# Optimization experiments

Measured on AMD Instinct MI355X. Metric: run time of the kernel, lower is better.

Reference implementation:

```python
import jax, jax.numpy as jnp
import numpy as np

MARGIN = 0.5
AP_VALUE = 0.8
AN_VALUE = 0.4
ABS_W = 1.0


def setup_inputs() -> dict:
    key = jax.random.key(0)
    k1, k2 = jax.random.split(key)
    bs, d = 16384, 64
    inputs = jax.random.normal(k1, (bs, d), dtype=jnp.float32)
    target = jax.random.randint(k2, (bs,), 0, 64, dtype=jnp.int64)
    return {"inputs": inputs, "target": target}


def reference(inputs, target):
    # L2-normalize features (normalize_feature=True)
    x = inputs / jnp.linalg.norm(inputs, axis=-1, keepdims=True)

    # cross-entropy on normalized features treated as logits
    logp = jax.nn.log_softmax(x, axis=-1)  # [bs, d]
    loss_ce = -jnp.mean(jnp.take_along_axis(logp, target[:, None], axis=1))

    # cosine-similarity matrix [bs, bs]
    dist = x @ x.T

    is_pos = target[None, :] == target[:, None]
    # hard mining: min similarity among positives, max among negatives (per row)
    dist_ap = jnp.min(jnp.where(is_pos, dist, jnp.inf), axis=1)   # [bs]
    dist_an = jnp.max(jnp.where(is_pos, -jnp.inf, dist), axis=1)  # [bs]

    loss = jnp.mean(jax.nn.relu(MARGIN + dist_ap - dist_an))

    # absolute (angular margin) terms
    abs_ap = jax.nn.relu(AP_VALUE - dist_ap)
    abs_an = jax.nn.relu(dist_an - AN_VALUE)
    loss = (jnp.mean(abs_an) + jnp.mean(abs_ap)) * ABS_W + loss

    return loss + loss_ce
```

## Files before the change

kernel.cpp:

```cpp
#include <hip/hip_runtime.h>


#define N_ROWS 16384
#define N_DIM 64

typedef __attribute__((ext_vector_type(8))) short bf16x8;
typedef __attribute__((ext_vector_type(4))) float f32x4;

__device__ inline unsigned short f2bf(float f) {
  unsigned u = __float_as_uint(f);
  unsigned r = u + 0x7fffu + ((u >> 16) & 1u);
  return (unsigned short)(r >> 16);
}

__device__ inline unsigned enc_key(float f) {
  unsigned u = __float_as_uint(f);
  return (u & 0x80000000u) ? ~u : (u | 0x80000000u);
}
__device__ inline float dec_key(unsigned k) {
  unsigned u = (k & 0x80000000u) ? (k ^ 0x80000000u) : ~k;
  return __uint_as_float(u);
}

__device__ inline void g2lds16(const void* g, void* l) {
  __builtin_amdgcn_global_load_lds(
      (const __attribute__((address_space(1))) void*)g,
      (__attribute__((address_space(3))) void*)l, 16, 0, 0);
}

__global__ void prep_kernel(const float* __restrict__ x, const int* __restrict__ tgt,
                            unsigned short* __restrict__ xb, float* __restrict__ ce_row,
                            unsigned* __restrict__ mp_key, unsigned* __restrict__ mn_key,
                            float* __restrict__ out) {
  const int row  = blockIdx.x * 4 + (threadIdx.x >> 6);
  const int lane = threadIdx.x & 63;
  float v  = x[row * N_DIM + lane];
  float ss = v * v;
#pragma unroll
  for (int s = 1; s < 64; s <<= 1) ss += __shfl_xor(ss, s, 64);
  float xn = v * rsqrtf(ss);
  xb[row * N_DIM + lane] = f2bf(xn);

  float e  = __expf(xn);
  float se = e;
#pragma unroll
  for (int s = 1; s < 64; s <<= 1) se += __shfl_xor(se, s, 64);
  float lse = __logf(se);
  int   t   = tgt[row];
  float xt  = __shfl(xn, t, 64);
  if (lane == 0) {
    ce_row[row] = lse - xt;
    mp_key[row] = 0xFFFFFFFFu;
    mn_key[row] = 0u;
  }
  if (blockIdx.x == 0 && threadIdx.x == 0) out[0] = 0.f;
}

__global__ __launch_bounds__(256, 8)
void mine_kernel(const unsigned short* __restrict__ xb, const int* __restrict__ tgt,
                 unsigned* __restrict__ mp_key, unsigned* __restrict__ mn_key) {
  __shared__ unsigned short Bt[2][4][1024];
  __shared__ unsigned short tjl[N_ROWS / 16];

  const int lane    = threadIdx.x & 63;
  const int wv      = threadIdx.x >> 6;
  const int iblk    = blockIdx.x >> 4;
  const int jspl    = blockIdx.x & 15;
  const int rowbase = iblk * 128 + wv * 32;
  const int m = lane & 15, q = lane >> 4;
  const int jbase = jspl * (N_ROWS / 16);

  bf16x8 a[2][2];
#pragma unroll
  for (int tr = 0; tr < 2; ++tr) {
    const unsigned short* p = xb + (rowbase + tr * 16 + m) * N_DIM + q * 8;
    a[tr][0] = *(const bf16x8*)(p);
    a[tr][1] = *(const bf16x8*)(p + 32);
  }
  int ti[2][4];
#pragma unroll
  for (int tr = 0; tr < 2; ++tr)
#pragma unroll
    for (int r = 0; r < 4; ++r)
      ti[tr][r] = tgt[rowbase + tr * 16 + q * 4 + r];

  float mp[8], mn[8];
#pragma unroll
  for (int k = 0; k < 8; ++k) { mp[k] = __builtin_inff(); mn[k] = -__builtin_inff(); }

  for (int k = threadIdx.x; k < N_ROWS / 16; k += 256)
    tjl[k] = (unsigned short)tgt[jbase + k];

  const unsigned short* src0 =
      xb + (jbase + (lane >> 3)) * N_DIM + (((lane & 7) ^ ((lane >> 3) & 7)) * 8);

#define STAGE(P_, BUF)                                                           \
  do {                                                                           \
    const unsigned short* s_ = src0 + ((P_) * 64 + wv * 16) * N_DIM;             \
    g2lds16(s_,             (unsigned short*)&Bt[(BUF)][wv][0] + lane * 8);      \
    g2lds16(s_ + 8 * N_DIM, (unsigned short*)&Bt[(BUF)][wv][0] + 512 + lane * 8);\
  } while (0)

  STAGE(0, 0);
  __syncthreads();

  const int roff0 = m * 128 + ((q * 16) ^ ((m & 7) << 4));
  const int roff1 = m * 128 + (((64) + q * 16) ^ ((m & 7) << 4));

  for (int ph = 0; ph < 16; ++ph) {
    const int pb = ph & 1;
    if (ph < 15) STAGE(ph + 1, pb ^ 1);
#pragma unroll 1
    for (int j4 = 0; j4 < 4; ++j4) {
      const int jc = ph * 4 + j4;
      const char* bb = (const char*)&Bt[pb][j4][0];
      const bf16x8 cb0 = *(const bf16x8*)(bb + roff0);
      const bf16x8 cb1 = *(const bf16x8*)(bb + roff1);
      const int    ctj = tjl[jc * 16 + m];

#pragma unroll
      for (int tr = 0; tr < 2; ++tr) {
        f32x4 acc = {0.f, 0.f, 0.f, 0.f};
        asm("s_nop 1\n\t"
            "v_mfma_f32_16x16x32_bf16 %0, %1, %2, %0"
            : "+v"(acc) : "v"(a[tr][0]), "v"(cb0));
        asm("v_mfma_f32_16x16x32_bf16 %0, %1, %2, %0\n\t"
            "s_nop 7\n\ts_nop 2"
            : "+v"(acc) : "v"(a[tr][1]), "v"(cb1));
#pragma unroll
        for (int r = 0; r < 4; ++r) {
          const bool  pos = (ctj == ti[tr][r]);
          const float d   = acc[r];
          const int   k   = tr * 4 + r;
          mp[k] = fminf(mp[k], pos ? d : __builtin_inff());
          mn[k] = fmaxf(mn[k], pos ? -__builtin_inff() : d);
        }
      }
    }
    __syncthreads();
  }
#undef STAGE

#pragma unroll
  for (int s = 1; s < 16; s <<= 1) {
#pragma unroll
    for (int k = 0; k < 8; ++k) {
      mp[k] = fminf(mp[k], __shfl_xor(mp[k], s, 64));
      mn[k] = fmaxf(mn[k], __shfl_xor(mn[k], s, 64));
    }
  }
  if (m == 0) {
#pragma unroll
    for (int tr = 0; tr < 2; ++tr)
#pragma unroll
      for (int r = 0; r < 4; ++r) {
        const int row = rowbase + tr * 16 + q * 4 + r;
        atomicMin(&mp_key[row], enc_key(mp[tr * 4 + r]));
        atomicMax(&mn_key[row], enc_key(mn[tr * 4 + r]));
      }
  }
}

__global__ void finalize_kernel(const unsigned* __restrict__ mp_key, const unsigned* __restrict__ mn_key,
                                const float* __restrict__ ce_row, float* __restrict__ out) {
  __shared__ float red[16];
  float s = 0.f;
#pragma unroll
  for (int it = 0; it < 2; ++it) {
    const int r = it * 8192 + blockIdx.x * 1024 + threadIdx.x;
    float ap = dec_key(mp_key[r]);
    float an = dec_key(mn_key[r]);
    s += fmaxf(0.5f + ap - an, 0.f) + fmaxf(0.8f - ap, 0.f) +
         fmaxf(an - 0.4f, 0.f) + ce_row[r];
  }
#pragma unroll
  for (int sh = 1; sh < 64; sh <<= 1) s += __shfl_xor(s, sh, 64);
  const int wv = threadIdx.x >> 6;
  if ((threadIdx.x & 63) == 0) red[wv] = s;
  __syncthreads();
  if (threadIdx.x == 0) {
    float t = 0.f;
#pragma unroll
    for (int w = 0; w < 16; ++w) t += red[w];
    atomicAdd(out, t * (1.0f / N_ROWS));
  }
}

extern "C" void kernel_launch(void* const* d_in, const int* in_sizes, int n_in,
                              void* d_out, int out_size, void* d_ws, size_t ws_size,
                              hipStream_t stream) {
  const float* x   = (const float*)d_in[0];
  const int*   tgt = (const int*)d_in[1];
  char* ws = (char*)d_ws;

  unsigned short* xb     = (unsigned short*)ws;
  unsigned*       mp_key = (unsigned*)(ws + (2u << 20));
  unsigned*       mn_key = (unsigned*)(ws + (2u << 20) + (64u << 10));
  float*          ce_row = (float*)(ws + (2u << 20) + (128u << 10));
  float*          out    = (float*)d_out;

  prep_kernel<<<N_ROWS / 4, 256, 0, stream>>>(x, tgt, xb, ce_row, mp_key, mn_key, out);
  mine_kernel<<<(N_ROWS / 128) * 16, 256, 0, stream>>>(xb, tgt, mp_key, mn_key);
  finalize_kernel<<<8, 1024, 0, stream>>>(mp_key, mn_key, ce_row, out);
}
```

Before: 162.9 us.

## Fold label masking into MFMA via one-hot augmented K dimension

The bf16 feature rows are extended from 64 to 128 columns, with a one-hot label block of +16 in the A copy and -16 in the B copy. The dot product therefore subtracts 256 for same-label pairs, so plain min and max over the augmented products give the hardest positive (offset by 256) and the hardest negative without per-element label compares. This removes the target loads and compare/select work from the inner loop. In exchange it doubles MFMA count, LDS traffic and global staging, drops the occupancy hint from 8 to 4, and assumes every row has a positive and that similarities stay within the offset gap.

```diff
diff --git a/kernel.cpp b/kernel.cpp
--- a/kernel.cpp
+++ b/kernel.cpp
@@ -2,7 +2,7 @@
 
 
 #define N_ROWS 16384
-#define N_DIM 64
+#define KDIM 128
 
 typedef __attribute__((ext_vector_type(8))) short bf16x8;
 typedef __attribute__((ext_vector_type(4))) float f32x4;
@@ -29,24 +29,29 @@
 }
 
 __global__ void prep_kernel(const float* __restrict__ x, const int* __restrict__ tgt,
-                            unsigned short* __restrict__ xb, float* __restrict__ ce_row,
+                            unsigned short* __restrict__ xbA, unsigned short* __restrict__ xbB,
+                            float* __restrict__ ce_row,
                             unsigned* __restrict__ mp_key, unsigned* __restrict__ mn_key,
                             float* __restrict__ out) {
   const int row  = blockIdx.x * 4 + (threadIdx.x >> 6);
   const int lane = threadIdx.x & 63;
-  float v  = x[row * N_DIM + lane];
+  float v  = x[row * 64 + lane];
   float ss = v * v;
 #pragma unroll
   for (int s = 1; s < 64; s <<= 1) ss += __shfl_xor(ss, s, 64);
   float xn = v * rsqrtf(ss);
-  xb[row * N_DIM + lane] = f2bf(xn);
+  int   t  = tgt[row];
+  const unsigned short b = f2bf(xn);
+  xbA[row * KDIM + lane] = b;
+  xbB[row * KDIM + lane] = b;
+  xbA[row * KDIM + 64 + lane] = (lane == t) ? (unsigned short)0x4180u : (unsigned short)0u;
+  xbB[row * KDIM + 64 + lane] = (lane == t) ? (unsigned short)0xC180u : (unsigned short)0u;
 
   float e  = __expf(xn);
   float se = e;
 #pragma unroll
   for (int s = 1; s < 64; s <<= 1) se += __shfl_xor(se, s, 64);
   float lse = __logf(se);
-  int   t   = tgt[row];
   float xt  = __shfl(xn, t, 64);
   if (lane == 0) {
     ce_row[row] = lse - xt;
@@ -56,11 +61,10 @@
   if (blockIdx.x == 0 && threadIdx.x == 0) out[0] = 0.f;
 }
 
-__global__ __launch_bounds__(256, 8)
-void mine_kernel(const unsigned short* __restrict__ xb, const int* __restrict__ tgt,
+__global__ __launch_bounds__(256, 4)
+void mine_kernel(const unsigned short* __restrict__ xbA, const unsigned short* __restrict__ xbB,
                  unsigned* __restrict__ mp_key, unsigned* __restrict__ mn_key) {
-  __shared__ unsigned short Bt[2][4][1024];
-  __shared__ unsigned short tjl[N_ROWS / 16];
+  __shared__ unsigned short Bt[2][4][2048];
 
   const int lane    = threadIdx.x & 63;
   const int wv      = threadIdx.x >> 6;
@@ -70,70 +74,61 @@
   const int m = lane & 15, q = lane >> 4;
   const int jbase = jspl * (N_ROWS / 16);
 
-  bf16x8 a[2][2];
+  bf16x8 a[2][4];
 #pragma unroll
   for (int tr = 0; tr < 2; ++tr) {
-    const unsigned short* p = xb + (rowbase + tr * 16 + m) * N_DIM + q * 8;
-    a[tr][0] = *(const bf16x8*)(p);
-    a[tr][1] = *(const bf16x8*)(p + 32);
-  }
-  int ti[2][4];
-#pragma unroll
-  for (int tr = 0; tr < 2; ++tr)
-#pragma unroll
-    for (int r = 0; r < 4; ++r)
-      ti[tr][r] = tgt[rowbase + tr * 16 + q * 4 + r];
+    const unsigned short* p = xbA + (rowbase + tr * 16 + m) * KDIM + q * 8;
+#pragma unroll
+    for (int ks = 0; ks < 4; ++ks) a[tr][ks] = *(const bf16x8*)(p + ks * 32);
+  }
 
   float mp[8], mn[8];
 #pragma unroll
   for (int k = 0; k < 8; ++k) { mp[k] = __builtin_inff(); mn[k] = -__builtin_inff(); }
 
-  for (int k = threadIdx.x; k < N_ROWS / 16; k += 256)
-    tjl[k] = (unsigned short)tgt[jbase + k];
-
-  const unsigned short* src0 =
-      xb + (jbase + (lane >> 3)) * N_DIM + (((lane & 7) ^ ((lane >> 3) & 7)) * 8);
-
-#define STAGE(P_, BUF)                                                           \
-  do {                                                                           \
-    const unsigned short* s_ = src0 + ((P_) * 64 + wv * 16) * N_DIM;             \
-    g2lds16(s_,             (unsigned short*)&Bt[(BUF)][wv][0] + lane * 8);      \
-    g2lds16(s_ + 8 * N_DIM, (unsigned short*)&Bt[(BUF)][wv][0] + 512 + lane * 8);\
+  const int ct   = wv * 4 + (lane >> 4);
+  const int gsel = (lane & 15) ^ ct;
+  const unsigned short* srcb = xbB + (jbase + ct) * KDIM + gsel * 8;
+
+#define STAGE(P_, BUF)                                                            \
+  do {                                                                            \
+    _Pragma("unroll")                                                             \
+    for (int ti = 0; ti < 4; ++ti)                                                \
+      g2lds16(srcb + ((P_) * 64 + ti * 16) * KDIM,                                \
+              (unsigned short*)&Bt[(BUF)][ti][0] + wv * 512 + lane * 8);          \
   } while (0)
 
   STAGE(0, 0);
   __syncthreads();
 
-  const int roff0 = m * 128 + ((q * 16) ^ ((m & 7) << 4));
-  const int roff1 = m * 128 + (((64) + q * 16) ^ ((m & 7) << 4));
+  int roff[4];
+#pragma unroll
+  for (int ks = 0; ks < 4; ++ks)
+    roff[ks] = m * 256 + ((ks * 64 + q * 16) ^ (m << 4));
 
   for (int ph = 0; ph < 16; ++ph) {
     const int pb = ph & 1;
     if (ph < 15) STAGE(ph + 1, pb ^ 1);
 #pragma unroll 1
     for (int j4 = 0; j4 < 4; ++j4) {
-      const int jc = ph * 4 + j4;
-      const char* bb = (const char*)&Bt[pb][j4][0];
-      const bf16x8 cb0 = *(const bf16x8*)(bb + roff0);
-      const bf16x8 cb1 = *(const bf16x8*)(bb + roff1);
-      const int    ctj = tjl[jc * 16 + m];
+      const char* tb = (const char*)&Bt[pb][j4][0];
+      const bf16x8 cb0 = *(const bf16x8*)(tb + roff[0]);
+      const bf16x8 cb1 = *(const bf16x8*)(tb + roff[1]);
+      const bf16x8 cb2 = *(const bf16x8*)(tb + roff[2]);
+      const bf16x8 cb3 = *(const bf16x8*)(tb + roff[3]);
 
 #pragma unroll
       for (int tr = 0; tr < 2; ++tr) {
         f32x4 acc = {0.f, 0.f, 0.f, 0.f};
-        asm("s_nop 1\n\t"
-            "v_mfma_f32_16x16x32_bf16 %0, %1, %2, %0"
-            : "+v"(acc) : "v"(a[tr][0]), "v"(cb0));
-        asm("v_mfma_f32_16x16x32_bf16 %0, %1, %2, %0\n\t"
-            "s_nop 7\n\ts_nop 2"
-            : "+v"(acc) : "v"(a[tr][1]), "v"(cb1));
+        acc = __builtin_amdgcn_mfma_f32_16x16x32_bf16(a[tr][0], cb0, acc, 0, 0, 0);
+        acc = __builtin_amdgcn_mfma_f32_16x16x32_bf16(a[tr][1], cb1, acc, 0, 0, 0);
+        acc = __builtin_amdgcn_mfma_f32_16x16x32_bf16(a[tr][2], cb2, acc, 0, 0, 0);
+        acc = __builtin_amdgcn_mfma_f32_16x16x32_bf16(a[tr][3], cb3, acc, 0, 0, 0);
 #pragma unroll
         for (int r = 0; r < 4; ++r) {
-          const bool  pos = (ctj == ti[tr][r]);
-          const float d   = acc[r];
-          const int   k   = tr * 4 + r;
-          mp[k] = fminf(mp[k], pos ? d : __builtin_inff());
-          mn[k] = fmaxf(mn[k], pos ? -__builtin_inff() : d);
+          const int k = tr * 4 + r;
+          mp[k] = fminf(mp[k], acc[r]);
+          mn[k] = fmaxf(mn[k], acc[r]);
         }
       }
     }
@@ -168,7 +163,7 @@
 #pragma unroll
   for (int it = 0; it < 2; ++it) {
     const int r = it * 8192 + blockIdx.x * 1024 + threadIdx.x;
-    float ap = dec_key(mp_key[r]);
+    float ap = dec_key(mp_key[r]) + 256.f;
     float an = dec_key(mn_key[r]);
     s += fmaxf(0.5f + ap - an, 0.f) + fmaxf(0.8f - ap, 0.f) +
          fmaxf(an - 0.4f, 0.f) + ce_row[r];
@@ -193,13 +188,14 @@
   const int*   tgt = (const int*)d_in[1];
   char* ws = (char*)d_ws;
 
-  unsigned short* xb     = (unsigned short*)ws;
-  unsigned*       mp_key = (unsigned*)(ws + (2u << 20));
-  unsigned*       mn_key = (unsigned*)(ws + (2u << 20) + (64u << 10));
-  float*          ce_row = (float*)(ws + (2u << 20) + (128u << 10));
+  unsigned short* xbA    = (unsigned short*)ws;
+  unsigned short* xbB    = (unsigned short*)(ws + (4u << 20));
+  unsigned*       mp_key = (unsigned*)(ws + (8u << 20));
+  unsigned*       mn_key = (unsigned*)(ws + (8u << 20) + (64u << 10));
+  float*          ce_row = (float*)(ws + (8u << 20) + (128u << 10));
   float*          out    = (float*)d_out;
 
-  prep_kernel<<<N_ROWS / 4, 256, 0, stream>>>(x, tgt, xb, ce_row, mp_key, mn_key, out);
-  mine_kernel<<<(N_ROWS / 128) * 16, 256, 0, stream>>>(xb, tgt, mp_key, mn_key);
+  prep_kernel<<<N_ROWS / 4, 256, 0, stream>>>(x, tgt, xbA, xbB, ce_row, mp_key, mn_key, out);
+  mine_kernel<<<(N_ROWS / 128) * 16, 256, 0, stream>>>(xbA, xbB, mp_key, mn_key);
   finalize_kernel<<<8, 1024, 0, stream>>>(mp_key, mn_key, ce_row, out);
 }
```

Result: faster. 143.4 us (median of 2 runs) (-12.0%).
